# Performance work log

Measured on AMD Instinct MI355X. Metric: run time of the kernel, lower is better.

Reference implementation:

```python
import jax, jax.numpy as jnp
import numpy as np

N_NODES = 100000
N_EDGES = 1600000
N_IN = 256
N_H = 128


def setup_inputs() -> dict:
    key = jax.random.key(0)
    k1, k2, k3, k4 = jax.random.split(key, 4)
    x = jax.random.normal(k1, (N_NODES, N_IN), dtype=jnp.float32)
    edge_index = jax.random.randint(k2, (2, N_EDGES), 0, N_NODES, dtype=jnp.int64)
    # GCNConv weights (glorot-like scale) and biases
    W1 = jax.random.normal(k3, (N_IN, N_H), dtype=jnp.float32) / np.sqrt(N_IN)
    b1 = jnp.zeros((N_H,), dtype=jnp.float32)
    W2 = jax.random.normal(k4, (N_H, N_H), dtype=jnp.float32) / np.sqrt(N_H)
    b2 = jnp.zeros((N_H,), dtype=jnp.float32)
    return {"x": x, "W1": W1, "b1": b1, "W2": W2, "b2": b2, "edge_index": edge_index}


def _gcn_conv(x, W, b, row, col, n_nodes):
    """PyG GCNConv: add self-loops, symmetric norm D^-1/2 A D^-1/2, aggregate at target (col)."""
    h = x @ W  # [N, out]
    # degree including self-loop (edge_weight = 1): deg[i] = 1 + #incoming edges at target i
    deg = jnp.ones((n_nodes,), dtype=x.dtype).at[col].add(1.0)
    dinv = jax.lax.rsqrt(deg)
    # off-diagonal edges: msg j->i weighted by dinv[j]*dinv[i]
    norm = dinv[row] * dinv[col]  # [E]
    msg = h[row] * norm[:, None]  # [E, out]
    agg = jax.ops.segment_sum(msg, col, num_segments=n_nodes)
    # self-loop contribution: weight dinv[i]^2
    agg = agg + h * (dinv * dinv)[:, None]
    return agg + b


def reference(x, W1, b1, W2, b2, edge_index):
    row, col = edge_index[0], edge_index[1]
    n = x.shape[0]
    out = jax.nn.relu(_gcn_conv(x, W1, b1, row, col, n))
    out = _gcn_conv(out, W2, b2, row, col, n)
    return out
```

## Files before the change

### kernel.cpp

```cpp
#include <hip/hip_runtime.h>


#define NN 100000
#define NH 128
#define NB 196
#define SB 256

__device__ __forceinline__ float bf2f(unsigned int u) { return __uint_as_float(u << 16); }
__device__ __forceinline__ unsigned short f2bf(float f) {
    unsigned int u = __float_as_uint(f);
    u = (u + 0x7fffu + ((u >> 16) & 1u)) >> 16;
    return (unsigned short)u;
}

__device__ __forceinline__ void dma16(const void* g, void* l) {
    __builtin_amdgcn_global_load_lds(
        (const __attribute__((address_space(1))) unsigned int*)g,
        (__attribute__((address_space(3))) unsigned int*)l, 16, 0, 0);
}

__global__ __launch_bounds__(256) void k_hist(const int* __restrict__ col,
                                              int* __restrict__ blockCnt, int E, int chb) {
    __shared__ int h[NB];
    int t = threadIdx.x, blk = blockIdx.x;
    if (t < NB) h[t] = 0;
    __syncthreads();
    int s = blk * chb, en = min(E, s + chb);
    for (int e = s + t; e < en; e += 256) atomicAdd(&h[col[e] >> 9], 1);
    __syncthreads();
    if (t < NB) blockCnt[t * SB + blk] = h[t];
}

__global__ __launch_bounds__(256) void k_base(const int* __restrict__ blockCnt,
                                              int* __restrict__ base) {
    __shared__ int s[256];
    int t = threadIdx.x;
    int tot = 0;
    if (t < NB)
        for (int j = 0; j < SB; ++j) tot += blockCnt[t * SB + j];
    s[t] = tot;
    __syncthreads();
    for (int off = 1; off < 256; off <<= 1) {
        int v = (t >= off) ? s[t - off] : 0;
        __syncthreads();
        s[t] += v;
        __syncthreads();
    }
    if (t < NB) base[t] = s[t] - tot;
    if (t == NB - 1) base[NB] = s[t];
}

__global__ __launch_bounds__(256) void k_bscan(const int* __restrict__ blockCnt,
                                               const int* __restrict__ base,
                                               int* __restrict__ blockOff) {
    __shared__ int s[256];
    int t = threadIdx.x, b = blockIdx.x;
    int v = blockCnt[b * SB + t];
    s[t] = v;
    __syncthreads();
    for (int off = 1; off < 256; off <<= 1) {
        int u = (t >= off) ? s[t - off] : 0;
        __syncthreads();
        s[t] += u;
        __syncthreads();
    }
    blockOff[b * SB + t] = base[b] + s[t] - v;
}

__global__ __launch_bounds__(256) void k_scatter(const int* __restrict__ row,
                                                 const int* __restrict__ col,
                                                 const int* __restrict__ blockOff,
                                                 unsigned int* __restrict__ pairs,
                                                 int E, int chb) {
    __shared__ int cur[NB];
    __shared__ int bof[NB];
    int t = threadIdx.x, blk = blockIdx.x;
    if (t < NB) {
        cur[t] = 0;
        bof[t] = blockOff[t * SB + blk];
    }
    __syncthreads();
    int s = blk * chb, en = min(E, s + chb);
    for (int e = s + t; e < en; e += 256) {
        int c = col[e];
        int b = c >> 9;
        int r = atomicAdd(&cur[b], 1);
        pairs[bof[b] + r] = (unsigned int)row[e] | ((unsigned int)(c & 511) << 17);
    }
}

__global__ __launch_bounds__(512) void k_bin(const unsigned int* __restrict__ pairs,
                                             const int* __restrict__ base,
                                             unsigned int* __restrict__ csr,
                                             int* __restrict__ offs,
                                             float* __restrict__ dinv, int n) {
    __shared__ int cnt[512];
    __shared__ int s[512];
    int t = threadIdx.x, b = blockIdx.x;
    cnt[t] = 0;
    __syncthreads();
    int e0 = base[b], e1 = base[b + 1];
    for (int i = e0 + t; i < e1; i += 512) atomicAdd(&cnt[pairs[i] >> 17], 1);
    __syncthreads();
    int v = cnt[t];
    int node = b * 512 + t;
    if (node < n) dinv[node] = rsqrtf(1.0f + (float)v);
    s[t] = v;
    __syncthreads();
    for (int off = 1; off < 512; off <<= 1) {
        int u = (t >= off) ? s[t - off] : 0;
        __syncthreads();
        s[t] += u;
        __syncthreads();
    }
    int excl = s[t] - v;
    if (node <= n) offs[node] = e0 + excl;
    __syncthreads();
    cnt[t] = e0 + excl;
    __syncthreads();
    for (int i = e0 + t; i < e1; i += 512) {
        unsigned int p = pairs[i];
        int d = atomicAdd(&cnt[p >> 17], 1);
        csr[d] = p & 0x1FFFFu;
    }
}

__global__ void k_wprep2(const float* __restrict__ W1, const float* __restrict__ W2,
                         unsigned short* __restrict__ T1, unsigned short* __restrict__ T2) {
    int idx = blockIdx.x * 256 + threadIdx.x;
    if (idx < 256 * 128) {
        int k = idx >> 7, c = idx & 127;
        T1[(size_t)c * 256 + k] = f2bf(W1[idx]);
    } else {
        int j = idx - 256 * 128;
        if (j < 128 * 128) {
            int k = j >> 7, c = j & 127;
            T2[(size_t)c * 128 + k] = f2bf(W2[j]);
        }
    }
}

template <int K>
__global__ __launch_bounds__(256) void k_gemm_mfma(const float* __restrict__ A,
                                                   const unsigned short* __restrict__ Bt,
                                                   const float* __restrict__ dinv,
                                                   unsigned short* __restrict__ C, int M) {
    using bf16x8 = __attribute__((ext_vector_type(8))) short;
    using f32x4  = __attribute__((ext_vector_type(4))) float;
    constexpr int T = K / 32;
    __shared__ uint4 sA[2][1024];
    __shared__ uint4 sB[2][512];

    const int lane = threadIdx.x & 63;
    const int wv   = threadIdx.x >> 6;
    const int r    = lane & 15;
    const int kb   = lane >> 4;
    const int rowBase = blockIdx.x * 128;

    auto stage = [&](int ks, int b) {
        const int kk = ks * 32;
#pragma unroll
        for (int c = 0; c < 4; ++c) {
            int sb = wv * 256 + c * 64;
            int q  = sb + lane;
            int row = q >> 3, pg = (q & 7) ^ (row & 7);
            int gr = rowBase + row; if (gr >= M) gr = M - 1;
            dma16(A + (size_t)gr * K + kk + pg * 4, &sA[b][sb]);
        }
#pragma unroll
        for (int c = 0; c < 2; ++c) {
            int sb = wv * 128 + c * 64;
            int q  = sb + lane;
            int bc = q >> 2, pg = (q & 3) ^ (bc & 3);
            dma16(Bt + (size_t)bc * K + kk + pg * 8, &sB[b][sb]);
        }
    };

    f32x4 acc[2][8];
#pragma unroll
    for (int m = 0; m < 2; ++m)
#pragma unroll
        for (int t = 0; t < 8; ++t) acc[m][t] = (f32x4){0.f, 0.f, 0.f, 0.f};

    stage(0, 0);
    __syncthreads();
#pragma unroll
    for (int ks = 0; ks < T; ++ks) {
        const int buf = ks & 1;
        if (ks + 1 < T) stage(ks + 1, buf ^ 1);
        bf16x8 ah[2];
#pragma unroll
        for (int m = 0; m < 2; ++m) {
            int rowl = wv * 32 + m * 16 + r;
            int p0 = (2 * kb)     ^ (rowl & 7);
            int p1 = (2 * kb + 1) ^ (rowl & 7);
            uint4 u0 = sA[buf][rowl * 8 + p0];
            uint4 u1 = sA[buf][rowl * 8 + p1];
            float f[8];
            *(uint4*)&f[0] = u0;
            *(uint4*)&f[4] = u1;
#pragma unroll
            for (int j = 0; j < 8; ++j) ah[m][j] = (short)f2bf(f[j]);
        }
#pragma unroll
        for (int t = 0; t < 8; ++t) {
            int bc = t * 16 + r;
            bf16x8 bh = *(const bf16x8*)&sB[buf][bc * 4 + (kb ^ (bc & 3))];
#pragma unroll
            for (int m = 0; m < 2; ++m)
                acc[m][t] = __builtin_amdgcn_mfma_f32_16x16x32_bf16(ah[m], bh, acc[m][t], 0, 0, 0);
        }
        __syncthreads();
    }
    const int wrow = rowBase + wv * 32;
#pragma unroll
    for (int m = 0; m < 2; ++m) {
#pragma unroll
        for (int q = 0; q < 4; ++q) {
            int orow = wrow + m * 16 + kb * 4 + q;
            if (orow < M) {
                float dv = dinv[orow];
#pragma unroll
                for (int t = 0; t < 8; ++t)
                    C[(size_t)orow * 128 + t * 16 + r] = f2bf(acc[m][t][q] * dv);
            }
        }
    }
}

template <int K>
__global__ __launch_bounds__(256) void k_gemm_bf16(const unsigned short* __restrict__ A,
                                                   const unsigned short* __restrict__ Bt,
                                                   const float* __restrict__ dinv,
                                                   unsigned short* __restrict__ C, int M) {
    using bf16x8 = __attribute__((ext_vector_type(8))) short;
    using f32x4  = __attribute__((ext_vector_type(4))) float;
    constexpr int T = K / 32;
    __shared__ uint4 sA[2][512];
    __shared__ uint4 sB[2][512];

    const int lane = threadIdx.x & 63;
    const int wv   = threadIdx.x >> 6;
    const int r    = lane & 15;
    const int kb   = lane >> 4;
    const int rowBase = blockIdx.x * 128;

    auto stage = [&](int ks, int b) {
        const int kk = ks * 32;
#pragma unroll
        for (int c = 0; c < 2; ++c) {
            int sb = wv * 128 + c * 64;
            int q  = sb + lane;
            int row = q >> 2, pg = (q & 3) ^ (row & 3);
            int gr = rowBase + row; if (gr >= M) gr = M - 1;
            dma16(A + (size_t)gr * K + kk + pg * 8, &sA[b][sb]);
        }
#pragma unroll
        for (int c = 0; c < 2; ++c) {
            int sb = wv * 128 + c * 64;
            int q  = sb + lane;
            int bc = q >> 2, pg = (q & 3) ^ (bc & 3);
            dma16(Bt + (size_t)bc * K + kk + pg * 8, &sB[b][sb]);
        }
    };

    f32x4 acc[2][8];
#pragma unroll
    for (int m = 0; m < 2; ++m)
#pragma unroll
        for (int t = 0; t < 8; ++t) acc[m][t] = (f32x4){0.f, 0.f, 0.f, 0.f};

    stage(0, 0);
    __syncthreads();
#pragma unroll
    for (int ks = 0; ks < T; ++ks) {
        const int buf = ks & 1;
        if (ks + 1 < T) stage(ks + 1, buf ^ 1);
        bf16x8 a[2];
#pragma unroll
        for (int m = 0; m < 2; ++m) {
            int rowl = wv * 32 + m * 16 + r;
            a[m] = *(const bf16x8*)&sA[buf][rowl * 4 + (kb ^ (rowl & 3))];
        }
#pragma unroll
        for (int t = 0; t < 8; ++t) {
            int bc = t * 16 + r;
            bf16x8 bh = *(const bf16x8*)&sB[buf][bc * 4 + (kb ^ (bc & 3))];
#pragma unroll
            for (int m = 0; m < 2; ++m)
                acc[m][t] = __builtin_amdgcn_mfma_f32_16x16x32_bf16(a[m], bh, acc[m][t], 0, 0, 0);
        }
        __syncthreads();
    }
    const int wrow = rowBase + wv * 32;
#pragma unroll
    for (int m = 0; m < 2; ++m) {
#pragma unroll
        for (int q = 0; q < 4; ++q) {
            int orow = wrow + m * 16 + kb * 4 + q;
            if (orow < M) {
                float dv = dinv[orow];
#pragma unroll
                for (int t = 0; t < 8; ++t)
                    C[(size_t)orow * 128 + t * 16 + r] = f2bf(acc[m][t][q] * dv);
            }
        }
    }
}

#define ACC8(u)                                              \
    a[0] += bf2f(u.x & 0xffffu); a[1] += bf2f(u.x >> 16);    \
    a[2] += bf2f(u.y & 0xffffu); a[3] += bf2f(u.y >> 16);    \
    a[4] += bf2f(u.z & 0xffffu); a[5] += bf2f(u.z >> 16);    \
    a[6] += bf2f(u.w & 0xffffu); a[7] += bf2f(u.w >> 16);

template <bool RELU, bool BF16OUT>
__global__ __launch_bounds__(256) void k_agg(const unsigned short* __restrict__ hb,
                                             const float* __restrict__ dinv,
                                             const int* __restrict__ off,
                                             const unsigned int* __restrict__ csr,
                                             const float* __restrict__ bias,
                                             void* __restrict__ outv, int n) {
    int gid  = blockIdx.x * 256 + threadIdx.x;
    int node = gid >> 4;
    int lane = gid & 15;
    if (node >= n) return;
    float di = dinv[node];
    uint4 us = *(const uint4*)(hb + ((size_t)node << 7) + lane * 8);
    float a[8];
    a[0] = bf2f(us.x & 0xffffu); a[1] = bf2f(us.x >> 16);
    a[2] = bf2f(us.y & 0xffffu); a[3] = bf2f(us.y >> 16);
    a[4] = bf2f(us.z & 0xffffu); a[5] = bf2f(us.z >> 16);
    a[6] = bf2f(us.w & 0xffffu); a[7] = bf2f(us.w >> 16);
    int e  = off[node];
    int e1 = off[node + 1];
    for (; e + 8 <= e1; e += 8) {
        unsigned int s0 = csr[e + 0], s1 = csr[e + 1], s2 = csr[e + 2], s3 = csr[e + 3];
        unsigned int s4 = csr[e + 4], s5 = csr[e + 5], s6 = csr[e + 6], s7 = csr[e + 7];
        uint4 u0 = *(const uint4*)(hb + ((size_t)s0 << 7) + lane * 8);
        uint4 u1 = *(const uint4*)(hb + ((size_t)s1 << 7) + lane * 8);
        uint4 u2 = *(const uint4*)(hb + ((size_t)s2 << 7) + lane * 8);
        uint4 u3 = *(const uint4*)(hb + ((size_t)s3 << 7) + lane * 8);
        uint4 u4 = *(const uint4*)(hb + ((size_t)s4 << 7) + lane * 8);
        uint4 u5 = *(const uint4*)(hb + ((size_t)s5 << 7) + lane * 8);
        uint4 u6 = *(const uint4*)(hb + ((size_t)s6 << 7) + lane * 8);
        uint4 u7 = *(const uint4*)(hb + ((size_t)s7 << 7) + lane * 8);
        ACC8(u0) ACC8(u1) ACC8(u2) ACC8(u3) ACC8(u4) ACC8(u5) ACC8(u6) ACC8(u7)
    }
    for (; e + 4 <= e1; e += 4) {
        unsigned int s0 = csr[e + 0], s1 = csr[e + 1], s2 = csr[e + 2], s3 = csr[e + 3];
        uint4 u0 = *(const uint4*)(hb + ((size_t)s0 << 7) + lane * 8);
        uint4 u1 = *(const uint4*)(hb + ((size_t)s1 << 7) + lane * 8);
        uint4 u2 = *(const uint4*)(hb + ((size_t)s2 << 7) + lane * 8);
        uint4 u3 = *(const uint4*)(hb + ((size_t)s3 << 7) + lane * 8);
        ACC8(u0) ACC8(u1) ACC8(u2) ACC8(u3)
    }
    for (; e < e1; ++e) {
        unsigned int s = csr[e];
        uint4 u = *(const uint4*)(hb + ((size_t)s << 7) + lane * 8);
        ACC8(u)
    }
    float4 b0 = *(const float4*)&bias[lane * 8];
    float4 b1 = *(const float4*)&bias[lane * 8 + 4];
    a[0] = a[0] * di + b0.x; a[1] = a[1] * di + b0.y;
    a[2] = a[2] * di + b0.z; a[3] = a[3] * di + b0.w;
    a[4] = a[4] * di + b1.x; a[5] = a[5] * di + b1.y;
    a[6] = a[6] * di + b1.z; a[7] = a[7] * di + b1.w;
    if (RELU) {
#pragma unroll
        for (int j = 0; j < 8; ++j) a[j] = fmaxf(a[j], 0.f);
    }
    if (BF16OUT) {
        uint4 o;
        o.x = (unsigned int)f2bf(a[0]) | ((unsigned int)f2bf(a[1]) << 16);
        o.y = (unsigned int)f2bf(a[2]) | ((unsigned int)f2bf(a[3]) << 16);
        o.z = (unsigned int)f2bf(a[4]) | ((unsigned int)f2bf(a[5]) << 16);
        o.w = (unsigned int)f2bf(a[6]) | ((unsigned int)f2bf(a[7]) << 16);
        *(uint4*)((unsigned short*)outv + ((size_t)node << 7) + lane * 8) = o;
    } else {
        float* op = (float*)outv + ((size_t)node << 7) + lane * 8;
        *(float4*)op       = make_float4(a[0], a[1], a[2], a[3]);
        *(float4*)(op + 4) = make_float4(a[4], a[5], a[6], a[7]);
    }
}

extern "C" void kernel_launch(void* const* d_in, const int* in_sizes, int n_in,
                              void* d_out, int out_size, void* d_ws, size_t ws_size,
                              hipStream_t stream) {
    const float* x  = (const float*)d_in[0];
    const float* W1 = (const float*)d_in[1];
    const float* b1 = (const float*)d_in[2];
    const float* W2 = (const float*)d_in[3];
    const float* b2 = (const float*)d_in[4];
    const int*   ei = (const int*)d_in[5];

    const int n = NN;
    const int E = in_sizes[5] / 2;
    const int* row = ei;
    const int* col = ei + E;

    char* ws = (char*)d_ws;
    size_t o = 0;
    auto alloc = [&](size_t bytes) {
        void* p = ws + o;
        o = (o + bytes + 255) & ~(size_t)255;
        return p;
    };
    int*            blockCnt = (int*)alloc((size_t)NB * SB * 4);
    int*            blockOff = (int*)alloc((size_t)NB * SB * 4);
    int*            base     = (int*)alloc((size_t)(NB + 1) * 4);
    int*            offs     = (int*)alloc((size_t)(n + 1) * 4);
    float*          dinv     = (float*)alloc((size_t)n * 4);
    unsigned int*   pairs    = (unsigned int*)alloc((size_t)E * 4);
    unsigned int*   csr      = (unsigned int*)alloc((size_t)E * 4);
    unsigned short* bufH     = (unsigned short*)alloc((size_t)n * NH * 2);
    unsigned short* bufG     = (unsigned short*)alloc((size_t)n * NH * 2);
    unsigned short* wt1      = (unsigned short*)alloc(256 * 128 * 2);
    unsigned short* wt2      = (unsigned short*)alloc(128 * 128 * 2);

    const int chb = (E + SB - 1) / SB;

    k_wprep2<<<(384 * 128 + 255) / 256, 256, 0, stream>>>(W1, W2, wt1, wt2);

    k_hist<<<SB, 256, 0, stream>>>(col, blockCnt, E, chb);
    k_base<<<1, 256, 0, stream>>>(blockCnt, base);
    k_bscan<<<NB, 256, 0, stream>>>(blockCnt, base, blockOff);
    k_scatter<<<SB, 256, 0, stream>>>(row, col, blockOff, pairs, E, chb);
    k_bin<<<NB, 512, 0, stream>>>(pairs, base, csr, offs, dinv, n);

    int aggBlocks  = (n + 15) / 16;
    int gemmBlocks = (n + 127) / 128;
    k_gemm_mfma<256><<<gemmBlocks, 256, 0, stream>>>(x, wt1, dinv, bufH, n);
    k_agg<true, true><<<aggBlocks, 256, 0, stream>>>(bufH, dinv, offs, csr, b1, bufG, n);
    k_gemm_bf16<128><<<gemmBlocks, 256, 0, stream>>>(bufG, wt2, dinv, bufH, n);
    k_agg<false, false><<<aggBlocks, 256, 0, stream>>>(bufH, dinv, offs, csr, b2, d_out, n);
}
```

Baseline: 225.2 us.

## Store hidden features in column-chunked layout so aggregation gathers stay cache-resident

GEMM epilogues now write the hidden features as 8 chunks of 16 columns each, and the second GEMM reads its A operand from that chunked layout. The aggregation kernel is rewritten so each block handles one 16-column chunk for 128 nodes, with two threads per node. This shrinks the working set of the random neighbor gathers so they fit better in L2/MALL, at the cost of reading the CSR index list eight times and doing smaller 32-byte gathers per edge.

```diff
diff --git a/kernel.cpp b/kernel.cpp
--- a/kernel.cpp
+++ b/kernel.cpp
@@ -222,7 +222,7 @@
                 float dv = dinv[orow];
 #pragma unroll
                 for (int t = 0; t < 8; ++t)
-                    C[(size_t)orow * 128 + t * 16 + r] = f2bf(acc[m][t][q] * dv);
+                    C[(size_t)t * M * 16 + (size_t)orow * 16 + r] = f2bf(acc[m][t][q] * dv);
             }
         }
     }
@@ -253,7 +253,8 @@
             int q  = sb + lane;
             int row = q >> 2, pg = (q & 3) ^ (row & 3);
             int gr = rowBase + row; if (gr >= M) gr = M - 1;
-            dma16(A + (size_t)gr * K + kk + pg * 8, &sA[b][sb]);
+            int ch = ks * 2 + (pg >> 1);
+            dma16(A + (size_t)ch * M * 16 + (size_t)gr * 16 + (pg & 1) * 8, &sA[b][sb]);
         }
 #pragma unroll
         for (int c = 0; c < 2; ++c) {
@@ -302,31 +303,32 @@
                 float dv = dinv[orow];
 #pragma unroll
                 for (int t = 0; t < 8; ++t)
-                    C[(size_t)orow * 128 + t * 16 + r] = f2bf(acc[m][t][q] * dv);
+                    C[(size_t)t * M * 16 + (size_t)orow * 16 + r] = f2bf(acc[m][t][q] * dv);
             }
         }
     }
 }
 
-#define ACC8(u)                                              \
+#define ACCC(u)                                              \
     a[0] += bf2f(u.x & 0xffffu); a[1] += bf2f(u.x >> 16);    \
     a[2] += bf2f(u.y & 0xffffu); a[3] += bf2f(u.y >> 16);    \
     a[4] += bf2f(u.z & 0xffffu); a[5] += bf2f(u.z >> 16);    \
     a[6] += bf2f(u.w & 0xffffu); a[7] += bf2f(u.w >> 16);
 
 template <bool RELU, bool BF16OUT>
-__global__ __launch_bounds__(256) void k_agg(const unsigned short* __restrict__ hb,
-                                             const float* __restrict__ dinv,
-                                             const int* __restrict__ off,
-                                             const unsigned int* __restrict__ csr,
-                                             const float* __restrict__ bias,
-                                             void* __restrict__ outv, int n) {
-    int gid  = blockIdx.x * 256 + threadIdx.x;
-    int node = gid >> 4;
-    int lane = gid & 15;
+__global__ __launch_bounds__(256) void k_aggc(const unsigned short* __restrict__ hc,
+                                              const float* __restrict__ dinv,
+                                              const int* __restrict__ off,
+                                              const unsigned int* __restrict__ csr,
+                                              const float* __restrict__ bias,
+                                              void* __restrict__ outv, int n) {
+    int chunk = blockIdx.x & 7;
+    int node  = (blockIdx.x >> 3) * 128 + (threadIdx.x >> 1);
+    int l2    = threadIdx.x & 1;
     if (node >= n) return;
+    const unsigned short* hb = hc + (size_t)chunk * n * 16;
     float di = dinv[node];
-    uint4 us = *(const uint4*)(hb + ((size_t)node << 7) + lane * 8);
+    uint4 us = *(const uint4*)(hb + (size_t)node * 16 + l2 * 8);
     float a[8];
     a[0] = bf2f(us.x & 0xffffu); a[1] = bf2f(us.x >> 16);
     a[2] = bf2f(us.y & 0xffffu); a[3] = bf2f(us.y >> 16);
@@ -337,31 +339,31 @@
     for (; e + 8 <= e1; e += 8) {
         unsigned int s0 = csr[e + 0], s1 = csr[e + 1], s2 = csr[e + 2], s3 = csr[e + 3];
         unsigned int s4 = csr[e + 4], s5 = csr[e + 5], s6 = csr[e + 6], s7 = csr[e + 7];
-        uint4 u0 = *(const uint4*)(hb + ((size_t)s0 << 7) + lane * 8);
-        uint4 u1 = *(const uint4*)(hb + ((size_t)s1 << 7) + lane * 8);
-        uint4 u2 = *(const uint4*)(hb + ((size_t)s2 << 7) + lane * 8);
-        uint4 u3 = *(const uint4*)(hb + ((size_t)s3 << 7) + lane * 8);
-        uint4 u4 = *(const uint4*)(hb + ((size_t)s4 << 7) + lane * 8);
-        uint4 u5 = *(const uint4*)(hb + ((size_t)s5 << 7) + lane * 8);
-        uint4 u6 = *(const uint4*)(hb + ((size_t)s6 << 7) + lane * 8);
-        uint4 u7 = *(const uint4*)(hb + ((size_t)s7 << 7) + lane * 8);
-        ACC8(u0) ACC8(u1) ACC8(u2) ACC8(u3) ACC8(u4) ACC8(u5) ACC8(u6) ACC8(u7)
+        uint4 u0 = *(const uint4*)(hb + (size_t)s0 * 16 + l2 * 8);
+        uint4 u1 = *(const uint4*)(hb + (size_t)s1 * 16 + l2 * 8);
+        uint4 u2 = *(const uint4*)(hb + (size_t)s2 * 16 + l2 * 8);
+        uint4 u3 = *(const uint4*)(hb + (size_t)s3 * 16 + l2 * 8);
+        uint4 u4 = *(const uint4*)(hb + (size_t)s4 * 16 + l2 * 8);
+        uint4 u5 = *(const uint4*)(hb + (size_t)s5 * 16 + l2 * 8);
+        uint4 u6 = *(const uint4*)(hb + (size_t)s6 * 16 + l2 * 8);
+        uint4 u7 = *(const uint4*)(hb + (size_t)s7 * 16 + l2 * 8);
+        ACCC(u0) ACCC(u1) ACCC(u2) ACCC(u3) ACCC(u4) ACCC(u5) ACCC(u6) ACCC(u7)
     }
     for (; e + 4 <= e1; e += 4) {
         unsigned int s0 = csr[e + 0], s1 = csr[e + 1], s2 = csr[e + 2], s3 = csr[e + 3];
-        uint4 u0 = *(const uint4*)(hb + ((size_t)s0 << 7) + lane * 8);
-        uint4 u1 = *(const uint4*)(hb + ((size_t)s1 << 7) + lane * 8);
-        uint4 u2 = *(const uint4*)(hb + ((size_t)s2 << 7) + lane * 8);
-        uint4 u3 = *(const uint4*)(hb + ((size_t)s3 << 7) + lane * 8);
-        ACC8(u0) ACC8(u1) ACC8(u2) ACC8(u3)
+        uint4 u0 = *(const uint4*)(hb + (size_t)s0 * 16 + l2 * 8);
+        uint4 u1 = *(const uint4*)(hb + (size_t)s1 * 16 + l2 * 8);
+        uint4 u2 = *(const uint4*)(hb + (size_t)s2 * 16 + l2 * 8);
+        uint4 u3 = *(const uint4*)(hb + (size_t)s3 * 16 + l2 * 8);
+        ACCC(u0) ACCC(u1) ACCC(u2) ACCC(u3)
     }
     for (; e < e1; ++e) {
         unsigned int s = csr[e];
-        uint4 u = *(const uint4*)(hb + ((size_t)s << 7) + lane * 8);
-        ACC8(u)
-    }
-    float4 b0 = *(const float4*)&bias[lane * 8];
-    float4 b1 = *(const float4*)&bias[lane * 8 + 4];
+        uint4 u = *(const uint4*)(hb + (size_t)s * 16 + l2 * 8);
+        ACCC(u)
+    }
+    float4 b0 = *(const float4*)&bias[chunk * 16 + l2 * 8];
+    float4 b1 = *(const float4*)&bias[chunk * 16 + l2 * 8 + 4];
     a[0] = a[0] * di + b0.x; a[1] = a[1] * di + b0.y;
     a[2] = a[2] * di + b0.z; a[3] = a[3] * di + b0.w;
     a[4] = a[4] * di + b1.x; a[5] = a[5] * di + b1.y;
@@ -376,9 +378,9 @@
         o.y = (unsigned int)f2bf(a[2]) | ((unsigned int)f2bf(a[3]) << 16);
         o.z = (unsigned int)f2bf(a[4]) | ((unsigned int)f2bf(a[5]) << 16);
         o.w = (unsigned int)f2bf(a[6]) | ((unsigned int)f2bf(a[7]) << 16);
-        *(uint4*)((unsigned short*)outv + ((size_t)node << 7) + lane * 8) = o;
+        *(uint4*)((unsigned short*)outv + (size_t)chunk * n * 16 + (size_t)node * 16 + l2 * 8) = o;
     } else {
-        float* op = (float*)outv + ((size_t)node << 7) + lane * 8;
+        float* op = (float*)outv + (size_t)node * 128 + chunk * 16 + l2 * 8;
         *(float4*)op       = make_float4(a[0], a[1], a[2], a[3]);
         *(float4*)(op + 4) = make_float4(a[4], a[5], a[6], a[7]);
     }
@@ -428,10 +430,10 @@
     k_scatter<<<SB, 256, 0, stream>>>(row, col, blockOff, pairs, E, chb);
     k_bin<<<NB, 512, 0, stream>>>(pairs, base, csr, offs, dinv, n);
 
-    int aggBlocks  = (n + 15) / 16;
+    int aggBlocks  = ((n + 127) / 128) * 8;
     int gemmBlocks = (n + 127) / 128;
     k_gemm_mfma<256><<<gemmBlocks, 256, 0, stream>>>(x, wt1, dinv, bufH, n);
-    k_agg<true, true><<<aggBlocks, 256, 0, stream>>>(bufH, dinv, offs, csr, b1, bufG, n);
+    k_aggc<true, true><<<aggBlocks, 256, 0, stream>>>(bufH, dinv, offs, csr, b1, bufG, n);
     k_gemm_bf16<128><<<gemmBlocks, 256, 0, stream>>>(bufG, wt2, dinv, bufH, n);
-    k_agg<false, false><<<aggBlocks, 256, 0, stream>>>(bufH, dinv, offs, csr, b2, d_out, n);
-}
+    k_aggc<false, false><<<aggBlocks, 256, 0, stream>>>(bufH, dinv, offs, csr, b2, d_out, n);
+}
```

Result: slower. 276.1 us (+22.6%).
